# Optimization experiments

Measured on AMD Instinct MI355X. Metric: run time of the kernel, lower is better.

Reference implementation:

```python
import jax, jax.numpy as jnp
import numpy as np

B, C_IN, H, W = 4, 256, 256, 256
L = 5000                 # candidate lines per image
N_PTS0, N_PTS1 = 32, 8   # sampled points per line, pooled points
DIM_LOI, DIM_FC = 128, 1024
N_OUT_LINE = 2500


def setup_inputs() -> dict:
    key = jax.random.key(0)
    ks = jax.random.split(key, 8)
    feature = jax.random.normal(ks[0], (B, C_IN, H, W), jnp.float32)
    # line endpoints in [0, 255) pixel coords (row, col)
    lines_in = jax.random.uniform(ks[1], (B, L, 2, 2), jnp.float32) * 255.0
    fc1_w = jax.random.normal(ks[2], (DIM_LOI, C_IN), jnp.float32) * 0.05
    fc1_b = jnp.zeros((DIM_LOI,), jnp.float32)
    w1 = jax.random.normal(ks[3], (DIM_FC, DIM_LOI * N_PTS1), jnp.float32) * 0.02
    b1 = jnp.zeros((DIM_FC,), jnp.float32)
    w2 = jax.random.normal(ks[4], (DIM_FC, DIM_FC), jnp.float32) * 0.02
    b2 = jnp.zeros((DIM_FC,), jnp.float32)
    w3 = jax.random.normal(ks[5], (4, DIM_FC), jnp.float32) * 0.02
    b3 = jnp.zeros((4,), jnp.float32)
    return dict(feature=feature, lines_in=lines_in, fc1_w=fc1_w, fc1_b=fc1_b,
                w1=w1, b1=b1, w2=w2, b2=b2, w3=w3, b3=b3)


def _bilinear_sample(xi, px, py):
    # xi: [C, H, W]; px, py: [P] float coords. Matches torch clamp(0, 255).
    px0 = jnp.clip(jnp.floor(px), 0.0, 255.0)
    py0 = jnp.clip(jnp.floor(py), 0.0, 255.0)
    px1 = jnp.clip(px0 + 1.0, 0.0, 255.0)
    py1 = jnp.clip(py0 + 1.0, 0.0, 255.0)
    px0l, py0l = px0.astype(jnp.int32), py0.astype(jnp.int32)
    px1l, py1l = px1.astype(jnp.int32), py1.astype(jnp.int32)
    xp = (xi[:, px0l, py0l] * (px1 - px) * (py1 - py)
          + xi[:, px1l, py0l] * (px - px0) * (py1 - py)
          + xi[:, px0l, py1l] * (px1 - px) * (py - py0)
          + xi[:, px1l, py1l] * (px - px0) * (py - py0))
    return xp  # [C, P]


def _select(p0, s0, m):
    # p0: [L,2,2], s0: [L,4], m: [L] bool. Threshold-masked, argsort by argmax
    # class (descending), cyclically padded to N_OUT_LINE.
    max_idx = jnp.argmax(s0, axis=1)
    sort_key = jnp.where(m, max_idx, -1)          # unmasked rows sink to the end
    order = jnp.argsort(-sort_key)                # stable, descending by class id
    cnt = m.sum()
    idxs = jnp.arange(N_OUT_LINE) % jnp.maximum(cnt, 1)
    sel = order[idxs]
    li = jnp.where(cnt > 0, p0[sel], jnp.zeros_like(p0[sel]))
    si = jnp.where(cnt > 0, s0[sel], jnp.zeros_like(s0[sel]))
    return li, si


def reference(feature, lines_in, fc1_w, fc1_b, w1, b1, w2, b2, w3, b3):
    # fc1: 1x1 conv -> [B, DIM_LOI, H, W]
    x = jnp.einsum('bchw,oc->bohw', feature, fc1_w) + fc1_b[None, :, None, None]

    # sample N_PTS0 points along each line: p0*lam + p1*(1-lam) - 0.5
    lam = jnp.linspace(0.0, 1.0, N_PTS0, dtype=jnp.float32)[:, None]  # [32,1]
    pts = lines_in[:, :, 0:1, :] * lam + lines_in[:, :, 1:2, :] * (1.0 - lam) - 0.5  # [B,L,32,2]
    px = pts[..., 0].reshape(B, -1)  # [B, L*32]
    py = pts[..., 1].reshape(B, -1)

    xp = jax.vmap(_bilinear_sample)(x, px, py)            # [B, C, L*32]
    xp = xp.reshape(B, DIM_LOI, L, N_PTS0).transpose(0, 2, 1, 3)  # [B, L, C, 32]

    # MaxPool1d(4, 4) over the point axis -> [B, L, C, 8]
    xp = xp.reshape(B, L, DIM_LOI, N_PTS1, N_PTS0 // N_PTS1).max(axis=-1)
    flat = xp.reshape(B, L, DIM_LOI * N_PTS1)

    # fc2 MLP: 1024 -> 1024 -> 1024 -> 4
    h = jax.nn.relu(jnp.einsum('blf,df->bld', flat, w1) + b1)
    h = jax.nn.relu(jnp.einsum('bld,ed->ble', h, w2) + b2)
    logits = jnp.einsum('ble,oe->blo', h, w3) + b3        # [B, L, 4]

    s = jax.nn.softmax(logits, axis=-1)
    mask = ((s[..., 1] > 0.25) | (s[..., 2] > 0.25) | (s[..., 3] > 0.25)) & (s[..., 0] < 0.25)

    lines_out, score_out = jax.vmap(_select)(lines_in, s, mask)
    return lines_out, score_out  # [B, 2500, 2, 2], [B, 2500, 4]
```

## Files before the change

### kernel.cpp

```cpp
#include <hip/hip_runtime.h>
#include <hip/hip_bf16.h>
#include <math.h>

#define BB 4
#define C_IN 256
#define HH 256
#define WW 256
#define LL 5000
#define N_PTS0 32
#define N_PTS1 8
#define DIM_LOI 128
#define DIM_FC 1024
#define N_OUT_LINE 2500
#define MM (BB * LL)
#define PIX (HH * WW)

typedef __attribute__((ext_vector_type(8))) short short8_t;
typedef __attribute__((ext_vector_type(4))) float float4v;

__device__ __forceinline__ short f2bf(float f) {
    union { float f; unsigned u; } c; c.f = f;
    unsigned u = c.u;
    u += 0x7FFFu + ((u >> 16) & 1u);
    return (short)(u >> 16);
}
__device__ __forceinline__ float bf2f(short h) {
    union { unsigned u; float f; } c; c.u = ((unsigned)(unsigned short)h) << 16;
    return c.f;
}

__device__ __forceinline__ void load_lds16(const void* g, void* l) {
    __builtin_amdgcn_global_load_lds(
        (const __attribute__((address_space(1))) void*)g,
        (__attribute__((address_space(3))) void*)l, 16, 0, 0);
}

__global__ __launch_bounds__(256) void conv_mfma_kernel(
    const float* __restrict__ feat,
    const short* __restrict__ whi,
    const short* __restrict__ wlo,
    const float* __restrict__ bias,
    float* __restrict__ x)
{
    __shared__ short As_hi[128][40];
    __shared__ short As_lo[128][40];
    __shared__ short Ws_hi[128][40];
    __shared__ short Ws_lo[128][40];

    const int t  = threadIdx.x;
    const int m0 = blockIdx.x * 128;
    const int b  = m0 >> 16;
    const int p0 = m0 & (PIX - 1);
    const float* fb = feat + (size_t)b * C_IN * PIX + p0;

    const int w = t >> 6, lane = t & 63;
    const int wmb = (w >> 1) * 64, wnb = (w & 1) * 64;
    const int fr = lane & 15;
    const int koff = (lane >> 4) << 3;

    const int sp = t & 127;
    const int cg = t >> 7;

    float4v acc[4][4];
#pragma unroll
    for (int mi = 0; mi < 4; mi++)
#pragma unroll
        for (int ni = 0; ni < 4; ni++)
            acc[mi][ni] = (float4v){0.f, 0.f, 0.f, 0.f};

    for (int k0 = 0; k0 < C_IN; k0 += 32) {
#pragma unroll
        for (int i = 0; i < 2; i++) {
            int idx = t + (i << 8);
            int row = idx >> 2;
            int kc  = (idx & 3) << 3;
            *(int4*)&Ws_hi[row][kc] = *(const int4*)(whi + row * C_IN + k0 + kc);
            *(int4*)&Ws_lo[row][kc] = *(const int4*)(wlo + row * C_IN + k0 + kc);
        }
#pragma unroll
        for (int j = 0; j < 8; j++) {
            int c = cg * 16 + j * 2;
            float v0 = fb[(size_t)(k0 + c) * PIX + sp];
            float v1 = fb[(size_t)(k0 + c + 1) * PIX + sp];
            short h0 = f2bf(v0), h1 = f2bf(v1);
            short l0 = f2bf(v0 - bf2f(h0)), l1 = f2bf(v1 - bf2f(h1));
            *(unsigned*)&As_hi[sp][c] =
                (unsigned)(unsigned short)h0 | ((unsigned)(unsigned short)h1 << 16);
            *(unsigned*)&As_lo[sp][c] =
                (unsigned)(unsigned short)l0 | ((unsigned)(unsigned short)l1 << 16);
        }
        __syncthreads();

        short8_t ah[4], al[4];
#pragma unroll
        for (int mi = 0; mi < 4; mi++) {
            ah[mi] = *(const short8_t*)&As_hi[wmb + mi * 16 + fr][koff];
            al[mi] = *(const short8_t*)&As_lo[wmb + mi * 16 + fr][koff];
        }
#pragma unroll
        for (int ni = 0; ni < 4; ni++) {
            short8_t bh = *(const short8_t*)&Ws_hi[wnb + ni * 16 + fr][koff];
            short8_t bl = *(const short8_t*)&Ws_lo[wnb + ni * 16 + fr][koff];
#pragma unroll
            for (int mi = 0; mi < 4; mi++) {
                acc[mi][ni] = __builtin_amdgcn_mfma_f32_16x16x32_bf16(
                    ah[mi], bh, acc[mi][ni], 0, 0, 0);
                acc[mi][ni] = __builtin_amdgcn_mfma_f32_16x16x32_bf16(
                    al[mi], bh, acc[mi][ni], 0, 0, 0);
                acc[mi][ni] = __builtin_amdgcn_mfma_f32_16x16x32_bf16(
                    ah[mi], bl, acc[mi][ni], 0, 0, 0);
            }
        }
        __syncthreads();
    }

#pragma unroll
    for (int ni = 0; ni < 4; ni++) {
        int ncol = wnb + ni * 16 + fr;
        float bv = bias[ncol];
#pragma unroll
        for (int mi = 0; mi < 4; mi++) {
            int r0 = m0 + wmb + mi * 16 + ((lane >> 4) << 2);
#pragma unroll
            for (int i2 = 0; i2 < 4; i2++) {
                x[(size_t)(r0 + i2) * 128 + ncol] = acc[mi][ni][i2] + bv;
            }
        }
    }
}

__global__ __launch_bounds__(128) void sample_pool_kernel(
    const float* __restrict__ lines,
    const float* __restrict__ x,
    short* __restrict__ phi,
    short* __restrict__ plo)
{
    const int bl = blockIdx.x;
    const int b  = bl / LL;
    const int c  = threadIdx.x;
    const float* lp = lines + (size_t)bl * 4;
    const float p0r = lp[0], p0c = lp[1], p1r = lp[2], p1c = lp[3];
    const float* xb = x + (size_t)b * PIX * 128;

    short8_t vh, vl;
#pragma unroll
    for (int g = 0; g < 8; g++) {
        float mx = -INFINITY;
#pragma unroll
        for (int j = 0; j < 4; j++) {
            int tt = g * 4 + j;
            float lam = (float)((double)tt / 31.0);
            float px = p0r * lam + p1r * (1.0f - lam) - 0.5f;
            float py = p0c * lam + p1c * (1.0f - lam) - 0.5f;
            float px0 = fminf(fmaxf(floorf(px), 0.0f), 255.0f);
            float py0 = fminf(fmaxf(floorf(py), 0.0f), 255.0f);
            float px1 = fminf(px0 + 1.0f, 255.0f);
            float py1 = fminf(py0 + 1.0f, 255.0f);
            int ix0 = (int)px0, iy0 = (int)py0, ix1 = (int)px1, iy1 = (int)py1;
            float wx1 = px1 - px, wx0 = px - px0;
            float wy1 = py1 - py, wy0 = py - py0;
            float v00 = xb[(size_t)(ix0 * WW + iy0) * 128 + c];
            float v10 = xb[(size_t)(ix1 * WW + iy0) * 128 + c];
            float v01 = xb[(size_t)(ix0 * WW + iy1) * 128 + c];
            float v11 = xb[(size_t)(ix1 * WW + iy1) * 128 + c];
            float v = v00 * (wx1 * wy1) + v10 * (wx0 * wy1)
                    + v01 * (wx1 * wy0) + v11 * (wx0 * wy0);
            mx = fmaxf(mx, v);
        }
        short h = f2bf(mx);
        vh[g] = h;
        vl[g] = f2bf(mx - bf2f(h));
    }
    *(short8_t*)(phi + (size_t)bl * 1024 + c * 8) = vh;
    *(short8_t*)(plo + (size_t)bl * 1024 + c * 8) = vl;
}

__global__ __launch_bounds__(256) void split_kernel(
    const float* __restrict__ w, short* __restrict__ hi, short* __restrict__ lo)
{
    const int i = (blockIdx.x * 256 + threadIdx.x) * 4;
    float4 v = *(const float4*)(w + i);
    float vv[4] = {v.x, v.y, v.z, v.w};
    short4 h, l;
    short hs[4], ls[4];
#pragma unroll
    for (int j = 0; j < 4; j++) {
        hs[j] = f2bf(vv[j]);
        ls[j] = f2bf(vv[j] - bf2f(hs[j]));
    }
    h.x = hs[0]; h.y = hs[1]; h.z = hs[2]; h.w = hs[3];
    l.x = ls[0]; l.y = ls[1]; l.z = ls[2]; l.w = ls[3];
    *(short4*)(hi + i) = h;
    *(short4*)(lo + i) = l;
}

template <bool SPLIT_OUT>
__global__ __launch_bounds__(256) void gemm_bf16x3(
    const short* __restrict__ Ahi, const short* __restrict__ Alo,
    const short* __restrict__ Bhi, const short* __restrict__ Blo,
    const float* __restrict__ bias,
    float* __restrict__ Cf, short* __restrict__ Chi, short* __restrict__ Clo,
    int M)
{
    __shared__ short lds[4][128 * 32];

    const int t = threadIdx.x;
    const int blk = blockIdx.x;
    const int tileM = (blk & 7) | ((blk >> 6) << 3);
    const int tileN = (blk >> 3) & 7;
    if (tileM * 128 >= M) return;
    const int m0 = tileM * 128, n0 = tileN * 128;
    const int w = t >> 6, lane = t & 63;
    const int wmb = (w >> 1) * 64, wnb = (w & 1) * 64;
    const int fr = lane & 15;
    const int koff = (lane >> 4) << 3;

    const short* mats[4] = {Ahi, Alo, Bhi, Blo};
    const short* gp[8];
    void* lp[8];
#pragma unroll
    for (int i = 0; i < 8; i++) {
        int row = i * 16 + (lane >> 2);
        int kc  = (lane & 3) * 8;
        int grow = (w < 2) ? min(m0 + row, M - 1) : (n0 + row);
        gp[i] = mats[w] + (size_t)grow * 1024 + kc;
        lp[i] = &lds[w][i * 512 + lane * 8];
    }

    float4v acc[4][4];
#pragma unroll
    for (int mi = 0; mi < 4; mi++)
#pragma unroll
        for (int ni = 0; ni < 4; ni++)
            acc[mi][ni] = (float4v){0.f, 0.f, 0.f, 0.f};

    for (int k0 = 0; k0 < 1024; k0 += 32) {
#pragma unroll
        for (int i = 0; i < 8; i++) {
            load_lds16(gp[i], lp[i]);
            gp[i] += 32;
        }
        __syncthreads();

        short8_t ah[4], al[4];
#pragma unroll
        for (int mi = 0; mi < 4; mi++) {
            int r = wmb + mi * 16 + fr;
            ah[mi] = *(const short8_t*)&lds[0][r * 32 + koff];
            al[mi] = *(const short8_t*)&lds[1][r * 32 + koff];
        }
#pragma unroll
        for (int ni = 0; ni < 4; ni++) {
            int r = wnb + ni * 16 + fr;
            short8_t bh = *(const short8_t*)&lds[2][r * 32 + koff];
            short8_t bl = *(const short8_t*)&lds[3][r * 32 + koff];
#pragma unroll
            for (int mi = 0; mi < 4; mi++) {
                acc[mi][ni] = __builtin_amdgcn_mfma_f32_16x16x32_bf16(
                    ah[mi], bh, acc[mi][ni], 0, 0, 0);
                acc[mi][ni] = __builtin_amdgcn_mfma_f32_16x16x32_bf16(
                    al[mi], bh, acc[mi][ni], 0, 0, 0);
                acc[mi][ni] = __builtin_amdgcn_mfma_f32_16x16x32_bf16(
                    ah[mi], bl, acc[mi][ni], 0, 0, 0);
            }
        }
        __syncthreads();
    }

#pragma unroll
    for (int ni = 0; ni < 4; ni++) {
        int ncol = n0 + wnb + ni * 16 + fr;
        float bv = bias[ncol];
#pragma unroll
        for (int mi = 0; mi < 4; mi++) {
            int r0 = m0 + wmb + mi * 16 + ((lane >> 4) << 2);
#pragma unroll
            for (int i2 = 0; i2 < 4; i2++) {
                int r = r0 + i2;
                if (r < M) {
                    float v = fmaxf(acc[mi][ni][i2] + bv, 0.0f);
                    if (SPLIT_OUT) {
                        short h = f2bf(v);
                        Chi[(size_t)r * 1024 + ncol] = h;
                        Clo[(size_t)r * 1024 + ncol] = f2bf(v - bf2f(h));
                    } else {
                        Cf[(size_t)r * 1024 + ncol] = v;
                    }
                }
            }
        }
    }
}

__global__ __launch_bounds__(256) void fc3_softmax_kernel(
    const float* __restrict__ h2, const float* __restrict__ w3,
    const float* __restrict__ b3, float* __restrict__ s, int* __restrict__ keys)
{
    const int m = blockIdx.x * 4 + (threadIdx.x >> 6);
    const int lane = threadIdx.x & 63;
    const float* hp = h2 + (size_t)m * DIM_FC;
    float a0 = 0.f, a1 = 0.f, a2 = 0.f, a3 = 0.f;
    for (int k = lane; k < DIM_FC; k += 64) {
        float hv = hp[k];
        a0 = fmaf(hv, w3[k], a0);
        a1 = fmaf(hv, w3[DIM_FC + k], a1);
        a2 = fmaf(hv, w3[2 * DIM_FC + k], a2);
        a3 = fmaf(hv, w3[3 * DIM_FC + k], a3);
    }
#pragma unroll
    for (int off = 32; off > 0; off >>= 1) {
        a0 += __shfl_down(a0, off, 64);
        a1 += __shfl_down(a1, off, 64);
        a2 += __shfl_down(a2, off, 64);
        a3 += __shfl_down(a3, off, 64);
    }
    if (lane == 0) {
        float l0 = a0 + b3[0], l1 = a1 + b3[1], l2 = a2 + b3[2], l3 = a3 + b3[3];
        float mxl = fmaxf(fmaxf(l0, l1), fmaxf(l2, l3));
        float e0 = expf(l0 - mxl), e1 = expf(l1 - mxl);
        float e2 = expf(l2 - mxl), e3 = expf(l3 - mxl);
        float inv = 1.0f / (e0 + e1 + e2 + e3);
        float s0 = e0 * inv, s1 = e1 * inv, s2 = e2 * inv, s3 = e3 * inv;
        float* sp = s + (size_t)m * 4;
        sp[0] = s0; sp[1] = s1; sp[2] = s2; sp[3] = s3;
        int best = 0; float bv = s0;
        if (s1 > bv) { best = 1; bv = s1; }
        if (s2 > bv) { best = 2; bv = s2; }
        if (s3 > bv) { best = 3; bv = s3; }
        bool msk = ((s1 > 0.25f) || (s2 > 0.25f) || (s3 > 0.25f)) && (s0 < 0.25f);
        keys[m] = msk ? best : -1;
    }
}

__global__ __launch_bounds__(64) void order_kernel(
    const int* __restrict__ keys, int* __restrict__ ord, int* __restrict__ cnts)
{
    const int b = blockIdx.x;
    const int lane = threadIdx.x;
    const int* kb = keys + b * LL;
    int c0 = 0, c1 = 0, c2 = 0, c3 = 0;
    for (int line = lane; line < LL; line += 64) {
        int k = kb[line];
        c0 += (k == 0); c1 += (k == 1); c2 += (k == 2); c3 += (k == 3);
    }
#pragma unroll
    for (int off = 32; off > 0; off >>= 1) {
        c0 += __shfl_down(c0, off, 64);
        c1 += __shfl_down(c1, off, 64);
        c2 += __shfl_down(c2, off, 64);
        c3 += __shfl_down(c3, off, 64);
    }
    int t0 = __shfl(c0, 0, 64), t1 = __shfl(c1, 0, 64);
    int t2 = __shfl(c2, 0, 64), t3 = __shfl(c3, 0, 64);
    if (lane == 0) cnts[b] = t0 + t1 + t2 + t3;
    int base[4];
    base[3] = 0; base[2] = t3; base[1] = t3 + t2; base[0] = t3 + t2 + t1;
    int run[4] = {0, 0, 0, 0};
    const unsigned long long below = (1ull << lane) - 1ull;
    int* ob = ord + b * LL;
    for (int s0 = 0; s0 < LL; s0 += 64) {
        int line = s0 + lane;
        int k = (line < LL) ? kb[line] : -2;
#pragma unroll
        for (int kk = 0; kk < 4; kk++) {
            unsigned long long mask = __ballot(k == kk);
            if (k == kk) {
                int pos = base[kk] + run[kk] + __popcll(mask & below);
                ob[pos] = line;
            }
            run[kk] += __popcll(mask);
        }
    }
}

__global__ __launch_bounds__(256) void fill_kernel(
    const float* __restrict__ lines, const float* __restrict__ s,
    const int* __restrict__ ord, const int* __restrict__ cnts,
    float* __restrict__ out)
{
    const int i = blockIdx.x * 256 + threadIdx.x;
    if (i >= BB * N_OUT_LINE) return;
    const int b = i / N_OUT_LINE;
    const int j = i % N_OUT_LINE;
    const int cnt = cnts[b];
    float4 lo = {0.f, 0.f, 0.f, 0.f}, sc = {0.f, 0.f, 0.f, 0.f};
    if (cnt > 0) {
        int line = ord[b * LL + (j % cnt)];
        lo = *(const float4*)(lines + ((size_t)b * LL + line) * 4);
        sc = *(const float4*)(s + ((size_t)b * LL + line) * 4);
    }
    *(float4*)(out + (size_t)i * 4) = lo;
    *(float4*)(out + (size_t)(BB * N_OUT_LINE) * 4 + (size_t)i * 4) = sc;
}

extern "C" void kernel_launch(void* const* d_in, const int* in_sizes, int n_in,
                              void* d_out, int out_size, void* d_ws, size_t ws_size,
                              hipStream_t stream) {
    (void)in_sizes; (void)n_in; (void)out_size; (void)ws_size;
    const float* feature = (const float*)d_in[0];
    const float* lines   = (const float*)d_in[1];
    const float* fc1_w   = (const float*)d_in[2];
    const float* fc1_b   = (const float*)d_in[3];
    const float* w1      = (const float*)d_in[4];
    const float* b1      = (const float*)d_in[5];
    const float* w2      = (const float*)d_in[6];
    const float* b2      = (const float*)d_in[7];
    const float* w3      = (const float*)d_in[8];
    const float* b3      = (const float*)d_in[9];
    float* out = (float*)d_out;

    float* x = (float*)d_ws;
    short* pooled_hi = (short*)(x + (size_t)BB * PIX * 128);
    short* pooled_lo = pooled_hi + (size_t)MM * DIM_FC;
    short* h1hi = (short*)x;
    short* h1lo = h1hi + (size_t)MM * DIM_FC;
    float* h2 = (float*)pooled_hi;
    short* w1hi = (short*)((char*)d_ws + 100u * 1024u * 1024u);
    short* w1lo = w1hi + DIM_FC * DIM_FC;
    short* w2hi = w1lo + DIM_FC * DIM_FC;
    short* w2lo = w2hi + DIM_FC * DIM_FC;
    float* s    = (float*)(pooled_lo + (size_t)MM * DIM_FC);
    int* keys   = (int*)(s + MM * 4);
    int* ord    = keys + MM;
    int* cnts   = ord + MM;
    short* fc1hi = (short*)(cnts + 64);
    short* fc1lo = fc1hi + DIM_LOI * C_IN;

    split_kernel<<<(DIM_LOI * C_IN) / 1024, 256, 0, stream>>>(fc1_w, fc1hi, fc1lo);
    conv_mfma_kernel<<<(BB * PIX) / 128, 256, 0, stream>>>(
        feature, fc1hi, fc1lo, fc1_b, x);
    sample_pool_kernel<<<MM, 128, 0, stream>>>(lines, x, pooled_hi, pooled_lo);
    split_kernel<<<DIM_FC * DIM_FC / 1024, 256, 0, stream>>>(w1, w1hi, w1lo);
    split_kernel<<<DIM_FC * DIM_FC / 1024, 256, 0, stream>>>(w2, w2hi, w2lo);

    const int mgroups = (((MM + 127) / 128) + 7) / 8;
    gemm_bf16x3<true><<<mgroups * 64, 256, 0, stream>>>(
        pooled_hi, pooled_lo, w1hi, w1lo, b1, nullptr, h1hi, h1lo, MM);
    gemm_bf16x3<false><<<mgroups * 64, 256, 0, stream>>>(
        h1hi, h1lo, w2hi, w2lo, b2, h2, nullptr, nullptr, MM);

    fc3_softmax_kernel<<<MM / 4, 256, 0, stream>>>(h2, w3, b3, s, keys);
    order_kernel<<<BB, 64, 0, stream>>>(keys, ord, cnts);
    fill_kernel<<<(BB * N_OUT_LINE + 255) / 256, 256, 0, stream>>>(
        lines, s, ord, cnts, out);
}
```

Measured before the change: 929.1 us.

## Rewrite fc2 bf16x3 GEMMs with triple-buffered LDS prefetch, swizzle and larger tiles

Replaces the two fc2 GEMMs with a 512-thread kernel that works on 256x128 tiles. It uses a three-stage LDS ring filled by direct global-to-LDS loads, and prefetches two k-steps ahead while running the MFMAs. It also adds an XOR swizzle on LDS columns to avoid bank conflicts, interleaves the prefetch with MFMA groups under s_setprio, and remaps the grid so blocks sharing an N tile are grouped. The aim is to hide global load latency and reduce barrier stalls in the dominant GEMMs. The cost is more LDS use, hand-placed waitcnt and barrier logic, and correctness that depends on the vmcnt counting.

After: 934.1 us. About the same (+0.5%).

```diff
diff --git a/kernel.cpp b/kernel.cpp
--- a/kernel.cpp
+++ b/kernel.cpp
@@ -35,6 +35,15 @@
         (__attribute__((address_space(3))) void*)l, 16, 0, 0);
 }
 
+__device__ __forceinline__ void wave_barrier() {
+    asm volatile("" ::: "memory");
+    __builtin_amdgcn_s_barrier();
+    asm volatile("" ::: "memory");
+}
+
+#define MFMA_B16(a, b, c) \
+    c = __builtin_amdgcn_mfma_f32_16x16x32_bf16(a, b, c, 0, 0, 0)
+
 __global__ __launch_bounds__(256) void conv_mfma_kernel(
     const float* __restrict__ feat,
     const short* __restrict__ whi,
@@ -103,12 +112,9 @@
             short8_t bl = *(const short8_t*)&Ws_lo[wnb + ni * 16 + fr][koff];
 #pragma unroll
             for (int mi = 0; mi < 4; mi++) {
-                acc[mi][ni] = __builtin_amdgcn_mfma_f32_16x16x32_bf16(
-                    ah[mi], bh, acc[mi][ni], 0, 0, 0);
-                acc[mi][ni] = __builtin_amdgcn_mfma_f32_16x16x32_bf16(
-                    al[mi], bh, acc[mi][ni], 0, 0, 0);
-                acc[mi][ni] = __builtin_amdgcn_mfma_f32_16x16x32_bf16(
-                    ah[mi], bl, acc[mi][ni], 0, 0, 0);
+                MFMA_B16(ah[mi], bh, acc[mi][ni]);
+                MFMA_B16(al[mi], bh, acc[mi][ni]);
+                MFMA_B16(ah[mi], bl, acc[mi][ni]);
             }
         }
         __syncthreads();
@@ -194,38 +200,60 @@
     *(short4*)(lo + i) = l;
 }
 
+#define NT 32
+#define BUF_SHORTS 24576
+
 template <bool SPLIT_OUT>
-__global__ __launch_bounds__(256) void gemm_bf16x3(
+__global__ __launch_bounds__(512, 2) void gemm_bf16x3_v3(
     const short* __restrict__ Ahi, const short* __restrict__ Alo,
     const short* __restrict__ Bhi, const short* __restrict__ Blo,
     const float* __restrict__ bias,
     float* __restrict__ Cf, short* __restrict__ Chi, short* __restrict__ Clo,
-    int M)
-{
-    __shared__ short lds[4][128 * 32];
-
-    const int t = threadIdx.x;
-    const int blk = blockIdx.x;
-    const int tileM = (blk & 7) | ((blk >> 6) << 3);
-    const int tileN = (blk >> 3) & 7;
-    if (tileM * 128 >= M) return;
-    const int m0 = tileM * 128, n0 = tileN * 128;
+    int M, int Mtiles)
+{
+    __shared__ short lds[3 * BUF_SHORTS];
+
+    const int t    = threadIdx.x;
+    const int bid  = blockIdx.x;
+    const int wgid  = (bid & 7) * Mtiles + (bid >> 3);
+    const int tileM = wgid >> 3;
+    const int tileN = wgid & 7;
+    const int m0 = tileM * 256, n0 = tileN * 128;
+
     const int w = t >> 6, lane = t & 63;
-    const int wmb = (w >> 1) * 64, wnb = (w & 1) * 64;
+    const int wmb = (w >> 1) * 64;
+    const int wnb = (w & 1) * 64;
     const int fr = lane & 15;
-    const int koff = (lane >> 4) << 3;
-
-    const short* mats[4] = {Ahi, Alo, Bhi, Blo};
-    const short* gp[8];
-    void* lp[8];
-#pragma unroll
-    for (int i = 0; i < 8; i++) {
-        int row = i * 16 + (lane >> 2);
-        int kc  = (lane & 3) * 8;
-        int grow = (w < 2) ? min(m0 + row, M - 1) : (n0 + row);
-        gp[i] = mats[w] + (size_t)grow * 1024 + kc;
-        lp[i] = &lds[w][i * 512 + lane * 8];
-    }
+    const int ksw = (((lane >> 4) ^ ((lane >> 1) & 3)) << 3);
+    const int a_base = (wmb + fr) * 32 + ksw;
+    const int b_base = 16384 + (wnb + fr) * 32 + ksw;
+
+    const short* gp[6];
+    int lp[6];
+    {
+        const int csrc = (lane & 3) ^ ((lane >> 3) & 3);
+#pragma unroll
+        for (int s = 0; s < 6; s++) {
+            int e = w * 6 + s;
+            int m_ = (e < 16) ? 0 : (e < 32) ? 1 : (e < 40) ? 2 : 3;
+            int j  = e - ((m_ == 0) ? 0 : (m_ == 1) ? 16 : (m_ == 2) ? 32 : 40);
+            const short* mp = (m_ == 0) ? Ahi : (m_ == 1) ? Alo
+                            : (m_ == 2) ? Bhi : Blo;
+            int mo = (m_ == 0) ? 0 : (m_ == 1) ? 8192
+                   : (m_ == 2) ? 16384 : 20480;
+            int row  = j * 16 + (lane >> 2);
+            int grow = (m_ < 2) ? min(m0 + row, M - 1) : (n0 + row);
+            gp[s] = mp + (size_t)grow * 1024 + csrc * 8;
+            lp[s] = mo + j * 512 + lane * 8;
+        }
+    }
+
+#pragma unroll
+    for (int s = 0; s < 6; s++) { load_lds16(gp[s], &lds[lp[s]]); gp[s] += 32; }
+#pragma unroll
+    for (int s = 0; s < 6; s++) { load_lds16(gp[s], &lds[BUF_SHORTS + lp[s]]); gp[s] += 32; }
+    asm volatile("s_waitcnt vmcnt(6)" ::: "memory");
+    wave_barrier();
 
     float4v acc[4][4];
 #pragma unroll
@@ -234,37 +262,62 @@
         for (int ni = 0; ni < 4; ni++)
             acc[mi][ni] = (float4v){0.f, 0.f, 0.f, 0.f};
 
-    for (int k0 = 0; k0 < 1024; k0 += 32) {
-#pragma unroll
-        for (int i = 0; i < 8; i++) {
-            load_lds16(gp[i], lp[i]);
-            gp[i] += 32;
-        }
-        __syncthreads();
-
-        short8_t ah[4], al[4];
-#pragma unroll
-        for (int mi = 0; mi < 4; mi++) {
-            int r = wmb + mi * 16 + fr;
-            ah[mi] = *(const short8_t*)&lds[0][r * 32 + koff];
-            al[mi] = *(const short8_t*)&lds[1][r * 32 + koff];
-        }
+    int off_cur = 0, off_nxt = BUF_SHORTS, off_pre = 2 * BUF_SHORTS;
+
+    for (int kt = 0; kt < NT; ++kt) {
+        const bool pf = (kt + 2 < NT);
+
+        short8_t bh[4], bl[4];
 #pragma unroll
         for (int ni = 0; ni < 4; ni++) {
-            int r = wnb + ni * 16 + fr;
-            short8_t bh = *(const short8_t*)&lds[2][r * 32 + koff];
-            short8_t bl = *(const short8_t*)&lds[3][r * 32 + koff];
-#pragma unroll
-            for (int mi = 0; mi < 4; mi++) {
-                acc[mi][ni] = __builtin_amdgcn_mfma_f32_16x16x32_bf16(
-                    ah[mi], bh, acc[mi][ni], 0, 0, 0);
-                acc[mi][ni] = __builtin_amdgcn_mfma_f32_16x16x32_bf16(
-                    al[mi], bh, acc[mi][ni], 0, 0, 0);
-                acc[mi][ni] = __builtin_amdgcn_mfma_f32_16x16x32_bf16(
-                    ah[mi], bl, acc[mi][ni], 0, 0, 0);
-            }
-        }
-        __syncthreads();
+            bh[ni] = *(const short8_t*)&lds[off_cur + b_base + ni * 512];
+            bl[ni] = *(const short8_t*)&lds[off_cur + b_base + ni * 512 + 4096];
+        }
+        short8_t ah = *(const short8_t*)&lds[off_cur + a_base];
+        short8_t al = *(const short8_t*)&lds[off_cur + a_base + 8192];
+        if (pf) {
+            load_lds16(gp[0], &lds[off_pre + lp[0]]); gp[0] += 32;
+            load_lds16(gp[1], &lds[off_pre + lp[1]]); gp[1] += 32;
+        }
+        wave_barrier();
+        asm volatile("s_waitcnt lgkmcnt(0)" ::: "memory");
+        __builtin_amdgcn_sched_barrier(0);
+        __builtin_amdgcn_s_setprio(1);
+#pragma unroll
+        for (int ni = 0; ni < 4; ni++) {
+            MFMA_B16(ah, bh[ni], acc[0][ni]);
+            MFMA_B16(al, bh[ni], acc[0][ni]);
+            MFMA_B16(ah, bl[ni], acc[0][ni]);
+        }
+        __builtin_amdgcn_s_setprio(0);
+        wave_barrier();
+
+#pragma unroll
+        for (int mi = 1; mi < 4; mi++) {
+            ah = *(const short8_t*)&lds[off_cur + a_base + mi * 512];
+            al = *(const short8_t*)&lds[off_cur + a_base + mi * 512 + 8192];
+            if (pf && mi < 3) {
+                load_lds16(gp[2 * mi],     &lds[off_pre + lp[2 * mi]]);     gp[2 * mi]     += 32;
+                load_lds16(gp[2 * mi + 1], &lds[off_pre + lp[2 * mi + 1]]); gp[2 * mi + 1] += 32;
+            }
+            wave_barrier();
+            asm volatile("s_waitcnt lgkmcnt(0)" ::: "memory");
+            __builtin_amdgcn_sched_barrier(0);
+            __builtin_amdgcn_s_setprio(1);
+#pragma unroll
+            for (int ni = 0; ni < 4; ni++) {
+                MFMA_B16(ah, bh[ni], acc[mi][ni]);
+                MFMA_B16(al, bh[ni], acc[mi][ni]);
+                MFMA_B16(ah, bl[ni], acc[mi][ni]);
+            }
+            __builtin_amdgcn_s_setprio(0);
+            if (mi < 3) wave_barrier();
+        }
+
+        if (pf) asm volatile("s_waitcnt vmcnt(6)" ::: "memory");
+        else    asm volatile("s_waitcnt vmcnt(0)" ::: "memory");
+        wave_barrier();
+        int tmp = off_cur; off_cur = off_nxt; off_nxt = off_pre; off_pre = tmp;
     }
 
 #pragma unroll
@@ -433,11 +486,11 @@
     split_kernel<<<DIM_FC * DIM_FC / 1024, 256, 0, stream>>>(w1, w1hi, w1lo);
     split_kernel<<<DIM_FC * DIM_FC / 1024, 256, 0, stream>>>(w2, w2hi, w2lo);
 
-    const int mgroups = (((MM + 127) / 128) + 7) / 8;
-    gemm_bf16x3<true><<<mgroups * 64, 256, 0, stream>>>(
-        pooled_hi, pooled_lo, w1hi, w1lo, b1, nullptr, h1hi, h1lo, MM);
-    gemm_bf16x3<false><<<mgroups * 64, 256, 0, stream>>>(
-        h1hi, h1lo, w2hi, w2lo, b2, h2, nullptr, nullptr, MM);
+    const int Mtiles = (MM + 255) / 256;
+    gemm_bf16x3_v3<true><<<Mtiles * 8, 512, 0, stream>>>(
+        pooled_hi, pooled_lo, w1hi, w1lo, b1, nullptr, h1hi, h1lo, MM, Mtiles);
+    gemm_bf16x3_v3<false><<<Mtiles * 8, 512, 0, stream>>>(
+        h1hi, h1lo, w2hi, w2lo, b2, h2, nullptr, nullptr, MM, Mtiles);
 
     fc3_softmax_kernel<<<MM / 4, 256, 0, stream>>>(h2, w3, b3, s, keys);
     order_kernel<<<BB, 64, 0, stream>>>(keys, ord, cnts);
```
